# Optimization experiments

Measured on AMD Instinct MI355X. Metric: run time of the kernel, lower is better.

Reference implementation:

```python
import jax, jax.numpy as jnp
import numpy as np

N, IN, H, M, D = 2048, 400, 256, 128, 8


def setup_inputs() -> dict:
    key = jax.random.key(0)
    ks = jax.random.split(key, 20)
    g = lambda k, shp, s: jax.random.normal(k, shp, jnp.float32) * s
    C = IN // 2
    return {
        "x": g(ks[0], (N, IN), 1.0),
        "memory": g(ks[1], (N, H, M), 1.0),
        "ke_w": g(ks[2], (H, C), 1.0 / np.sqrt(C)),
        "ke_b": g(ks[3], (H,), 0.01),
        "km_w": g(ks[4], (M, H), 1.0 / np.sqrt(H)),
        "km_b": g(ks[5], (M,), 0.01),
        "kw2_w": g(ks[6], (D, H), 1.0 / np.sqrt(H)),
        "kw2_b": g(ks[7], (D,), 0.01),
        "sum_w": g(ks[8], (H, 2 * H), 1.0 / np.sqrt(2 * H)),
        "sum_b": g(ks[9], (H,), 0.01),
        "out_w": g(ks[10], (1, H), 1.0 / np.sqrt(H)),
        "out_b": g(ks[11], (1,), 0.01),
        "ve_w": g(ks[12], (H, IN), 1.0 / np.sqrt(IN)),
        "ve_b": g(ks[13], (H,), 0.01),
        "er_w": g(ks[14], (D, H, H), 1.0 / np.sqrt(H)),
        "er_b": g(ks[15], (D, H), 0.01),
        "ad_w": g(ks[16], (D, H, H), 1.0 / np.sqrt(H)),
        "ad_b": g(ks[17], (D, H), 0.01),
    }


def reference(x, memory, ke_w, ke_b, km_w, km_b, kw2_w, kw2_b,
              sum_w, sum_b, out_w, out_b, ve_w, ve_b,
              er_w, er_b, ad_w, ad_b):
    n, c2 = x.shape
    c = c2 // 2
    # query = sum of the two halves of x
    q = x.reshape(n, 2, c).sum(axis=1)                       # (N, C)
    k = q @ ke_w.T + ke_b                                    # (N, H)
    w = jax.nn.softmax(k @ km_w.T + km_b, axis=-1)           # (N, M) read/write weights
    w2 = jax.nn.softmax(k @ kw2_w.T + kw2_b, axis=-1)        # (N, D) expert gates
    # memory read: weighted sum over memory slots
    r = jnp.einsum('nhm,nm->nh', memory, w)                  # (N, H)
    f = jnp.tanh(jnp.concatenate([k, r], axis=1) @ sum_w.T + sum_b)
    y = f @ out_w.T + out_b                                  # (N, 1)
    v = x @ ve_w.T + ve_b                                    # (N, H)
    # DynamicLinear: gate-weighted mixture of per-expert linear maps
    # (fused: avoids materializing per-sample (N,H,H) weights)
    e = jax.nn.sigmoid(jnp.einsum('ni,doi,nd->no', v, er_w, w2) + w2 @ er_b)
    a = jnp.tanh(jnp.einsum('ni,doi,nd->no', v, ad_w, w2) + w2 @ ad_b)
    # memory write: erase then add
    memory = memory * (1.0 - w[:, None, :] * e[:, :, None])
    memory = memory + w[:, None, :] * a[:, :, None]
    return y, memory
```

## Files before the change

### kernel.cpp

```cpp
#include <hip/hip_runtime.h>
#include <math.h>

#define N_  2048
#define IN_ 400
#define C_  200
#define H_  256
#define M_  128
#define D_  8

#define KQ   224
#define KX   416
#define KBIG 2176
#define NZ   4
#define KSPL (KBIG / NZ)
#define KS   512

typedef __bf16 bf16x8 __attribute__((ext_vector_type(8)));
typedef float  f32x4  __attribute__((ext_vector_type(4)));

__device__ __forceinline__ ushort f2bf(float x) { __bf16 b = (__bf16)x; return __builtin_bit_cast(ushort, b); }
__device__ __forceinline__ float  bf2f(ushort u) { unsigned v = ((unsigned)u) << 16; return __builtin_bit_cast(float, v); }

#define P0 212992
#define P1 (P0 + 114688)
#define P2 (P1 + 81920)
#define P3 (P2 + 278528)
#define WC_KE (256 * KQ)
#define WC_VE (WC_KE + 256 * KX)
#define WC_SW (WC_VE + 256 * 512)
#define WC_KM (WC_SW + 128 * 256)
__global__ __launch_bounds__(256) void prep_all_kernel(
    const float* __restrict__ x,
    const float* __restrict__ ke, const float* __restrict__ ve,
    const float* __restrict__ sw, const float* __restrict__ km,
    const float* __restrict__ er_w, const float* __restrict__ er_b,
    const float* __restrict__ ad_w, const float* __restrict__ ad_b,
    ushort* __restrict__ x_bf, ushort* __restrict__ q_bf,
    ushort* __restrict__ wout, ushort* __restrict__ wcat)
{
    int idx = blockIdx.x * 256 + threadIdx.x;
    ushort pk[4];
    if (idx < P0) {
        int n = idx / (KX / 4), g = idx % (KX / 4), c0 = g * 4;
#pragma unroll
        for (int j = 0; j < 4; j++) {
            int c = c0 + j;
            pk[j] = f2bf((c < IN_) ? x[(size_t)n * IN_ + c] : 0.f);
        }
        *(ushort4*)&x_bf[(size_t)n * KX + c0] = *(ushort4*)pk;
    } else if (idx < P1) {
        int i = idx - P0;
        int n = i / (KQ / 4), g = i % (KQ / 4), c0 = g * 4;
#pragma unroll
        for (int j = 0; j < 4; j++) {
            int c = c0 + j;
            pk[j] = f2bf((c < C_) ? x[(size_t)n * IN_ + c] + x[(size_t)n * IN_ + C_ + c] : 0.f);
        }
        *(ushort4*)&q_bf[(size_t)n * KQ + c0] = *(ushort4*)pk;
    } else if (idx < P2) {
        int s0 = (idx - P1) * 4;
#pragma unroll
        for (int j = 0; j < 4; j++) {
            int s = s0 + j;
            float val;
            if (s < WC_KE)      { int r = s / KQ, c = s % KQ; val = (c < C_) ? ke[r * C_ + c] : 0.f; }
            else if (s < WC_VE) { int i = s - WC_KE; int r = i / KX, c = i % KX; val = (c < IN_) ? ve[r * IN_ + c] : 0.f; }
            else if (s < WC_SW) { val = sw[s - WC_VE]; }
            else                { val = km[s - WC_SW]; }
            pk[j] = f2bf(val);
        }
        *(ushort4*)&wout[s0] = *(ushort4*)pk;
    } else {
        int i = idx - P2;
        int o = i / (KBIG / 4), g = i % (KBIG / 4), c0 = g * 4;
        const float* Wsrc = (o < 256) ? er_w : ad_w;
        const float* bsrc = (o < 256) ? er_b : ad_b;
        int oo = o & 255;
#pragma unroll
        for (int j = 0; j < 4; j++) {
            int c = c0 + j;
            float val = 0.f;
            if (c < 2048)      { int d = c >> 8, ii = c & 255; val = Wsrc[(size_t)(d * 256 + oo) * 256 + ii]; }
            else if (c < 2056) { val = bsrc[(c - 2048) * 256 + oo]; }
            pk[j] = f2bf(val);
        }
        *(ushort4*)&wcat[(size_t)o * KBIG + c0] = *(ushort4*)pk;
    }
}

template<int ACT, int OUTBF>
__global__ __launch_bounds__(256) void gemm_mfma(
    const ushort* __restrict__ A, int lda,
    const ushort* __restrict__ B, int ldb,
    const float* __restrict__ bias,
    void* __restrict__ Cv, int ldc, size_t csplit, int ksplit)
{
    constexpr int BM = 128, BN = 64;
    __shared__ ushort As[BM][40];
    __shared__ ushort Bs[BN][40];
    const int tid = threadIdx.x, lane = tid & 63, wave = tid >> 6;
    const int wm = (wave >> 1) * 64, wn = (wave & 1) * 32;
    const int m0 = blockIdx.y * BM, n0 = blockIdx.x * BN;
    const int kFrom = blockIdx.z * ksplit, kTo = kFrom + ksplit;

    f32x4 acc[4][2] = {};
    const int sr = tid >> 2;
    const int sc = (tid & 3) * 8;

    for (int k0 = kFrom; k0 < kTo; k0 += 32) {
        uint4 a0 = *(const uint4*)&A[(size_t)(m0 + sr) * lda + k0 + sc];
        uint4 a1 = *(const uint4*)&A[(size_t)(m0 + sr + 64) * lda + k0 + sc];
        uint4 b0 = *(const uint4*)&B[(size_t)(n0 + sr) * ldb + k0 + sc];
        *(uint4*)&As[sr][sc] = a0;
        *(uint4*)&As[sr + 64][sc] = a1;
        *(uint4*)&Bs[sr][sc] = b0;
        __syncthreads();

        const int ko = (lane >> 4) * 8;
        bf16x8 af[4], bfr[2];
#pragma unroll
        for (int i = 0; i < 4; i++)
            af[i] = __builtin_bit_cast(bf16x8, *(const uint4*)&As[wm + i * 16 + (lane & 15)][ko]);
#pragma unroll
        for (int j = 0; j < 2; j++)
            bfr[j] = __builtin_bit_cast(bf16x8, *(const uint4*)&Bs[wn + j * 16 + (lane & 15)][ko]);
#pragma unroll
        for (int i = 0; i < 4; i++)
#pragma unroll
            for (int j = 0; j < 2; j++)
                acc[i][j] = __builtin_amdgcn_mfma_f32_16x16x32_bf16(af[i], bfr[j], acc[i][j], 0, 0, 0);
        __syncthreads();
    }

    float* Cf = (float*)Cv + blockIdx.z * csplit;
    ushort* Cb = (ushort*)Cv;
#pragma unroll
    for (int i = 0; i < 4; i++) {
#pragma unroll
        for (int j = 0; j < 2; j++) {
            int row = m0 + wm + i * 16 + (lane >> 4) * 4;
            int col = n0 + wn + j * 16 + (lane & 15);
#pragma unroll
            for (int r = 0; r < 4; r++) {
                float val = acc[i][j][r];
                if (bias) val += bias[col];
                if (ACT == 1) val = tanhf(val);
                if (OUTBF) Cb[(size_t)(row + r) * ldc + col] = f2bf(val);
                else       Cf[(size_t)(row + r) * ldc + col] = val;
            }
        }
    }
}

__global__ __launch_bounds__(256) void vw_kernel(
    const ushort* __restrict__ kr, const float* __restrict__ v,
    const float* __restrict__ kw2_w, const float* __restrict__ kw2_b,
    ushort* __restrict__ vw)
{
    __shared__ float kf[H_], vl[H_], lg[8], w2l[8];
    const int n = blockIdx.x, t = threadIdx.x;
    if (t < 64) {
        ushort4 u = ((const ushort4*)(kr + (size_t)n * KS))[t];
        kf[t * 4 + 0] = bf2f(u.x); kf[t * 4 + 1] = bf2f(u.y);
        kf[t * 4 + 2] = bf2f(u.z); kf[t * 4 + 3] = bf2f(u.w);
        float4 vv = ((const float4*)(v + (size_t)n * H_))[t];
        vl[t * 4 + 0] = vv.x; vl[t * 4 + 1] = vv.y;
        vl[t * 4 + 2] = vv.z; vl[t * 4 + 3] = vv.w;
    }
    __syncthreads();
    {
        int d = t >> 5, l = t & 31;
        float acc = 0.f;
        const float* wr = kw2_w + d * H_;
#pragma unroll
        for (int s = 0; s < 8; s++) acc += kf[l + 32 * s] * wr[l + 32 * s];
#pragma unroll
        for (int off = 16; off; off >>= 1) acc += __shfl_xor(acc, off);
        if (l == 0) lg[d] = acc + kw2_b[d];
    }
    __syncthreads();
    if (t < 8) {
        float val = lg[t];
        float mx = val;
#pragma unroll
        for (int off = 1; off < 8; off <<= 1) mx = fmaxf(mx, __shfl_xor(mx, off));
        float e = expf(val - mx), s = e;
#pragma unroll
        for (int off = 1; off < 8; off <<= 1) s += __shfl_xor(s, off);
        w2l[t] = e / s;
    }
    __syncthreads();
    ushort* row = vw + (size_t)n * KBIG;
    for (int g = t; g < KBIG / 4; g += 256) {
        int c0 = g * 4;
        ushort pk[4];
#pragma unroll
        for (int j = 0; j < 4; j++) {
            int c = c0 + j;
            float val = 0.f;
            if (c < 2048)      val = w2l[c >> 8] * vl[c & 255];
            else if (c < 2056) val = w2l[c - 2048];
            pk[j] = f2bf(val);
        }
        *(ushort4*)&row[c0] = *(ushort4*)pk;
    }
}

__global__ __launch_bounds__(256) void mem_stream_kernel(
    const float* __restrict__ mem_in,
    const float* __restrict__ wlog,
    const float* __restrict__ parts,
    float* __restrict__ mem_out,
    ushort* __restrict__ kr)
{
    __shared__ float wl[M_];
    __shared__ float el[128], al[128];
    __shared__ float red[4];
    const int n = blockIdx.x >> 1, half = blockIdx.x & 1, hbase = half * 128;
    const int t = threadIdx.x;

    const int col = (t < 128) ? (hbase + t) : (256 + hbase + (t - 128));
    float pacc = 0.f;
#pragma unroll
    for (int z = 0; z < NZ; z++)
        pacc += parts[(size_t)z * N_ * 512 + (size_t)n * 512 + col];

    float lv = 0.f;
    if (t < 128) {
        lv = wlog[(size_t)n * M_ + t];
        float mx = lv;
#pragma unroll
        for (int off = 32; off; off >>= 1) mx = fmaxf(mx, __shfl_xor(mx, off));
        if ((t & 63) == 0) red[t >> 6] = mx;
        el[t] = 1.f / (1.f + expf(-pacc));
    } else {
        al[t - 128] = tanhf(pacc);
    }
    __syncthreads();
    if (t < 128) {
        float gmax = fmaxf(red[0], red[1]);
        float ev = expf(lv - gmax);
        float s = ev;
#pragma unroll
        for (int off = 32; off; off >>= 1) s += __shfl_xor(s, off);
        if ((t & 63) == 0) red[2 + (t >> 6)] = s;
        wl[t] = ev;
    }
    __syncthreads();
    if (t < 128) wl[t] *= 1.f / (red[2] + red[3]);
    __syncthreads();

    const int wave = t >> 6, lane = t & 63, half2 = lane >> 5, l32 = lane & 31;
    const float4* min4 = (const float4*)(mem_in + ((size_t)n * H_ + hbase) * M_);
    float4* mout4 = (float4*)(mem_out + ((size_t)n * H_ + hbase) * M_);
    float4 wv = ((const float4*)wl)[l32];
#pragma unroll 4
    for (int i = 0; i < 16; i++) {
        int hl = i * 8 + wave * 2 + half2;
        float4 mv = min4[hl * 32 + l32];
        float eh = el[hl], ah = al[hl];
        float4 nv;
        nv.x = mv.x * (1.f - wv.x * eh) + wv.x * ah;
        nv.y = mv.y * (1.f - wv.y * eh) + wv.y * ah;
        nv.z = mv.z * (1.f - wv.z * eh) + wv.z * ah;
        nv.w = mv.w * (1.f - wv.w * eh) + wv.w * ah;
        mout4[hl * 32 + l32] = nv;
        float racc = mv.x * wv.x + mv.y * wv.y + mv.z * wv.z + mv.w * wv.w;
#pragma unroll
        for (int off = 1; off < 32; off <<= 1) racc += __shfl_xor(racc, off);
        if (l32 == 0) kr[(size_t)n * KS + H_ + hbase + hl] = f2bf(racc);
    }
}

__global__ void y_kernel(const float* __restrict__ f, const float* __restrict__ out_w,
                         const float* __restrict__ out_b, float* __restrict__ y) {
    int n = blockIdx.x, t = threadIdx.x;
    float acc = 0.f;
#pragma unroll
    for (int j = 0; j < 4; j++) acc += f[(size_t)n * H_ + t + j * 64] * out_w[t + j * 64];
#pragma unroll
    for (int off = 32; off; off >>= 1) acc += __shfl_xor(acc, off);
    if (t == 0) y[n] = acc + out_b[0];
}

extern "C" void kernel_launch(void* const* d_in, const int* in_sizes, int n_in,
                              void* d_out, int out_size, void* d_ws, size_t ws_size,
                              hipStream_t stream) {
    const float* x      = (const float*)d_in[0];
    const float* mem_in = (const float*)d_in[1];
    const float* ke_w   = (const float*)d_in[2];
    const float* ke_b   = (const float*)d_in[3];
    const float* km_w   = (const float*)d_in[4];
    const float* km_b   = (const float*)d_in[5];
    const float* kw2_w  = (const float*)d_in[6];
    const float* kw2_b  = (const float*)d_in[7];
    const float* sum_w  = (const float*)d_in[8];
    const float* sum_b  = (const float*)d_in[9];
    const float* out_w  = (const float*)d_in[10];
    const float* out_b  = (const float*)d_in[11];
    const float* ve_w   = (const float*)d_in[12];
    const float* ve_b   = (const float*)d_in[13];
    const float* er_w   = (const float*)d_in[14];
    const float* er_b   = (const float*)d_in[15];
    const float* ad_w   = (const float*)d_in[16];
    const float* ad_b   = (const float*)d_in[17];

    float* y_out   = (float*)d_out;
    float* mem_out = (float*)d_out + N_;

    float* ws = (float*)d_ws;
    size_t o = 0;
    float*  parts  = ws + o;            o += (size_t)NZ * N_ * 512;
    ushort* vw     = (ushort*)(ws + o); o += (size_t)N_ * KBIG / 2;
    ushort* Wcat   = (ushort*)(ws + o); o += (size_t)512 * KBIG / 2;
    ushort* kr     = (ushort*)(ws + o); o += (size_t)N_ * KS / 2;
    ushort* x_bf   = (ushort*)(ws + o); o += (size_t)N_ * KX / 2;
    ushort* q_bf   = (ushort*)(ws + o); o += (size_t)N_ * KQ / 2;
    ushort* wbf    = (ushort*)(ws + o); o += (size_t)WC_KM / 2;
    float*  v      = ws + o;            o += (size_t)N_ * H_;
    float*  wlog   = ws + o;            o += (size_t)N_ * M_;
    float*  fbuf   = (float*)x_bf;

    ushort* ke_bf  = wbf;
    ushort* ve_bf  = wbf + WC_KE;
    ushort* sum_bf = wbf + WC_VE;
    ushort* km_bf  = wbf + WC_SW;

    prep_all_kernel<<<P3 / 256, 256, 0, stream>>>(
        x, ke_w, ve_w, sum_w, km_w, er_w, er_b, ad_w, ad_b, x_bf, q_bf, wbf, Wcat);
    gemm_mfma<0, 1><<<dim3(H_ / 64, N_ / 128, 1), 256, 0, stream>>>(
        q_bf, KQ, ke_bf, KQ, ke_b, kr, KS, 0, KQ);
    gemm_mfma<0, 0><<<dim3(H_ / 64, N_ / 128, 1), 256, 0, stream>>>(
        x_bf, KX, ve_bf, KX, ve_b, v, H_, 0, KX);
    vw_kernel<<<N_, 256, 0, stream>>>(kr, v, kw2_w, kw2_b, vw);
    gemm_mfma<0, 0><<<dim3(512 / 64, N_ / 128, NZ), 256, 0, stream>>>(
        vw, KBIG, Wcat, KBIG, nullptr, parts, 512, (size_t)N_ * 512, KSPL);
    gemm_mfma<0, 0><<<dim3(M_ / 64, N_ / 128, 1), 256, 0, stream>>>(
        kr, KS, km_bf, H_, km_b, wlog, M_, 0, H_);
    mem_stream_kernel<<<2 * N_, 256, 0, stream>>>(mem_in, wlog, parts, mem_out, kr);
    gemm_mfma<1, 0><<<dim3(H_ / 64, N_ / 128, 1), 256, 0, stream>>>(
        kr, KS, sum_bf, KS, sum_b, fbuf, H_, 0, KS);
    y_kernel<<<N_, 64, 0, stream>>>(fbuf, out_w, out_b, y_out);
}
```

Before: 203.6 us.

## Double-buffer GEMM core, merge GEMM launches, fuse sum-GEMM with output head

Moves the MFMA GEMM into a shared device function with double-buffered LDS tiles, so global loads for the next K-slice overlap compute on the current one. The ke/ve GEMMs share one launch, the big expert GEMM shares one with the km logits GEMM, and the sum GEMM is fused with tanh and the out_w dot into a single kernel that writes y directly. The memory-stream kernel switches to vector math with nontemporal loads and stores. This cuts launch count and the intermediate f buffer, at the cost of more LDS per block and some idle z-slice blocks in the merged launch.

```diff
diff --git a/kernel.cpp b/kernel.cpp
--- a/kernel.cpp
+++ b/kernel.cpp
@@ -88,51 +88,59 @@
     }
 }
 
-template<int ACT, int OUTBF>
-__global__ __launch_bounds__(256) void gemm_mfma(
+__device__ __forceinline__ void gemm_core_128x64(
     const ushort* __restrict__ A, int lda,
     const ushort* __restrict__ B, int ldb,
     const float* __restrict__ bias,
-    void* __restrict__ Cv, int ldc, size_t csplit, int ksplit)
-{
-    constexpr int BM = 128, BN = 64;
-    __shared__ ushort As[BM][40];
-    __shared__ ushort Bs[BN][40];
+    void* __restrict__ Cv, int ldc, int outbf,
+    int m0, int n0, int kFrom, int kTo,
+    ushort (*As)[128][40], ushort (*Bs)[64][40])
+{
     const int tid = threadIdx.x, lane = tid & 63, wave = tid >> 6;
     const int wm = (wave >> 1) * 64, wn = (wave & 1) * 32;
-    const int m0 = blockIdx.y * BM, n0 = blockIdx.x * BN;
-    const int kFrom = blockIdx.z * ksplit, kTo = kFrom + ksplit;
+    const int sr = tid >> 2, sc = (tid & 3) * 8;
 
     f32x4 acc[4][2] = {};
-    const int sr = tid >> 2;
-    const int sc = (tid & 3) * 8;
-
-    for (int k0 = kFrom; k0 < kTo; k0 += 32) {
-        uint4 a0 = *(const uint4*)&A[(size_t)(m0 + sr) * lda + k0 + sc];
-        uint4 a1 = *(const uint4*)&A[(size_t)(m0 + sr + 64) * lda + k0 + sc];
-        uint4 b0 = *(const uint4*)&B[(size_t)(n0 + sr) * ldb + k0 + sc];
-        *(uint4*)&As[sr][sc] = a0;
-        *(uint4*)&As[sr + 64][sc] = a1;
-        *(uint4*)&Bs[sr][sc] = b0;
-        __syncthreads();
-
+
+    auto compute = [&](int b) {
         const int ko = (lane >> 4) * 8;
         bf16x8 af[4], bfr[2];
 #pragma unroll
         for (int i = 0; i < 4; i++)
-            af[i] = __builtin_bit_cast(bf16x8, *(const uint4*)&As[wm + i * 16 + (lane & 15)][ko]);
+            af[i] = __builtin_bit_cast(bf16x8, *(const uint4*)&As[b][wm + i * 16 + (lane & 15)][ko]);
 #pragma unroll
         for (int j = 0; j < 2; j++)
-            bfr[j] = __builtin_bit_cast(bf16x8, *(const uint4*)&Bs[wn + j * 16 + (lane & 15)][ko]);
+            bfr[j] = __builtin_bit_cast(bf16x8, *(const uint4*)&Bs[b][wn + j * 16 + (lane & 15)][ko]);
 #pragma unroll
         for (int i = 0; i < 4; i++)
 #pragma unroll
             for (int j = 0; j < 2; j++)
                 acc[i][j] = __builtin_amdgcn_mfma_f32_16x16x32_bf16(af[i], bfr[j], acc[i][j], 0, 0, 0);
+    };
+
+    uint4 a0 = *(const uint4*)&A[(size_t)(m0 + sr) * lda + kFrom + sc];
+    uint4 a1 = *(const uint4*)&A[(size_t)(m0 + sr + 64) * lda + kFrom + sc];
+    uint4 b0 = *(const uint4*)&B[(size_t)(n0 + sr) * ldb + kFrom + sc];
+    *(uint4*)&As[0][sr][sc] = a0;
+    *(uint4*)&As[0][sr + 64][sc] = a1;
+    *(uint4*)&Bs[0][sr][sc] = b0;
+    __syncthreads();
+
+    int cur = 0;
+    for (int k0 = kFrom + 32; k0 < kTo; k0 += 32) {
+        a0 = *(const uint4*)&A[(size_t)(m0 + sr) * lda + k0 + sc];
+        a1 = *(const uint4*)&A[(size_t)(m0 + sr + 64) * lda + k0 + sc];
+        b0 = *(const uint4*)&B[(size_t)(n0 + sr) * ldb + k0 + sc];
+        compute(cur);
+        *(uint4*)&As[cur ^ 1][sr][sc] = a0;
+        *(uint4*)&As[cur ^ 1][sr + 64][sc] = a1;
+        *(uint4*)&Bs[cur ^ 1][sr][sc] = b0;
         __syncthreads();
-    }
-
-    float* Cf = (float*)Cv + blockIdx.z * csplit;
+        cur ^= 1;
+    }
+    compute(cur);
+
+    float* Cf = (float*)Cv;
     ushort* Cb = (ushort*)Cv;
 #pragma unroll
     for (int i = 0; i < 4; i++) {
@@ -144,11 +152,46 @@
             for (int r = 0; r < 4; r++) {
                 float val = acc[i][j][r];
                 if (bias) val += bias[col];
-                if (ACT == 1) val = tanhf(val);
-                if (OUTBF) Cb[(size_t)(row + r) * ldc + col] = f2bf(val);
+                if (outbf) Cb[(size_t)(row + r) * ldc + col] = f2bf(val);
                 else       Cf[(size_t)(row + r) * ldc + col] = val;
             }
         }
+    }
+}
+
+__global__ __launch_bounds__(256) void kv_kernel(
+    const ushort* __restrict__ q_bf, const ushort* __restrict__ ke_bf,
+    const float* __restrict__ ke_b, ushort* __restrict__ kr,
+    const ushort* __restrict__ x_bf, const ushort* __restrict__ ve_bf,
+    const float* __restrict__ ve_b, float* __restrict__ v)
+{
+    __shared__ ushort As[2][128][40];
+    __shared__ ushort Bs[2][64][40];
+    if (blockIdx.z == 0)
+        gemm_core_128x64(q_bf, KQ, ke_bf, KQ, ke_b, kr, KS, 1,
+                         blockIdx.y * 128, blockIdx.x * 64, 0, KQ, As, Bs);
+    else
+        gemm_core_128x64(x_bf, KX, ve_bf, KX, ve_b, v, H_, 0,
+                         blockIdx.y * 128, blockIdx.x * 64, 0, KX, As, Bs);
+}
+
+__global__ __launch_bounds__(256) void bigw_kernel(
+    const ushort* __restrict__ vw, const ushort* __restrict__ Wcat,
+    float* __restrict__ parts,
+    const ushort* __restrict__ kr, const ushort* __restrict__ km_bf,
+    const float* __restrict__ km_b, float* __restrict__ wlog)
+{
+    __shared__ ushort As[2][128][40];
+    __shared__ ushort Bs[2][64][40];
+    const int z = blockIdx.z;
+    if (z < NZ) {
+        gemm_core_128x64(vw, KBIG, Wcat, KBIG, nullptr,
+                         parts + (size_t)z * N_ * 512, 512, 0,
+                         blockIdx.y * 128, blockIdx.x * 64, z * KSPL, (z + 1) * KSPL, As, Bs);
+    } else {
+        if (blockIdx.x >= 2) return;
+        gemm_core_128x64(kr, KS, km_bf, H_, km_b, wlog, M_, 0,
+                         blockIdx.y * 128, blockIdx.x * 64, 0, H_, As, Bs);
     }
 }
 
@@ -251,36 +294,119 @@
     __syncthreads();
 
     const int wave = t >> 6, lane = t & 63, half2 = lane >> 5, l32 = lane & 31;
-    const float4* min4 = (const float4*)(mem_in + ((size_t)n * H_ + hbase) * M_);
-    float4* mout4 = (float4*)(mem_out + ((size_t)n * H_ + hbase) * M_);
-    float4 wv = ((const float4*)wl)[l32];
+    const f32x4* min4 = (const f32x4*)(mem_in + ((size_t)n * H_ + hbase) * M_);
+    f32x4* mout4 = (f32x4*)(mem_out + ((size_t)n * H_ + hbase) * M_);
+    f32x4 wv = ((const f32x4*)wl)[l32];
 #pragma unroll 4
     for (int i = 0; i < 16; i++) {
         int hl = i * 8 + wave * 2 + half2;
-        float4 mv = min4[hl * 32 + l32];
+        f32x4 mv = __builtin_nontemporal_load(&min4[hl * 32 + l32]);
         float eh = el[hl], ah = al[hl];
-        float4 nv;
-        nv.x = mv.x * (1.f - wv.x * eh) + wv.x * ah;
-        nv.y = mv.y * (1.f - wv.y * eh) + wv.y * ah;
-        nv.z = mv.z * (1.f - wv.z * eh) + wv.z * ah;
-        nv.w = mv.w * (1.f - wv.w * eh) + wv.w * ah;
-        mout4[hl * 32 + l32] = nv;
-        float racc = mv.x * wv.x + mv.y * wv.y + mv.z * wv.z + mv.w * wv.w;
+        f32x4 nv = mv * (1.f - wv * eh) + wv * ah;
+        __builtin_nontemporal_store(nv, &mout4[hl * 32 + l32]);
+        float racc = mv[0] * wv[0] + mv[1] * wv[1] + mv[2] * wv[2] + mv[3] * wv[3];
 #pragma unroll
         for (int off = 1; off < 32; off <<= 1) racc += __shfl_xor(racc, off);
         if (l32 == 0) kr[(size_t)n * KS + H_ + hbase + hl] = f2bf(racc);
     }
 }
 
-__global__ void y_kernel(const float* __restrict__ f, const float* __restrict__ out_w,
-                         const float* __restrict__ out_b, float* __restrict__ y) {
-    int n = blockIdx.x, t = threadIdx.x;
-    float acc = 0.f;
-#pragma unroll
-    for (int j = 0; j < 4; j++) acc += f[(size_t)n * H_ + t + j * 64] * out_w[t + j * 64];
-#pragma unroll
-    for (int off = 32; off; off >>= 1) acc += __shfl_xor(acc, off);
-    if (t == 0) y[n] = acc + out_b[0];
+__global__ __launch_bounds__(256) void fy_kernel(
+    const ushort* __restrict__ kr, const ushort* __restrict__ sum_bf,
+    const float* __restrict__ sum_b, const float* __restrict__ out_w,
+    const float* __restrict__ out_b, float* __restrict__ y)
+{
+    __shared__ ushort As[2][64][40];
+    __shared__ ushort Bs[2][256][40];
+    __shared__ float yl[64][4];
+    const int tid = threadIdx.x, lane = tid & 63, wave = tid >> 6;
+    const int wn = wave * 64;
+    const int m0 = blockIdx.x * 64;
+    const int sr = tid >> 2, sc = (tid & 3) * 8;
+
+    f32x4 acc[4][4] = {};
+
+    auto compute = [&](int b) {
+        const int ko = (lane >> 4) * 8;
+        bf16x8 af[4], bfr[4];
+#pragma unroll
+        for (int i = 0; i < 4; i++)
+            af[i] = __builtin_bit_cast(bf16x8, *(const uint4*)&As[b][i * 16 + (lane & 15)][ko]);
+#pragma unroll
+        for (int j = 0; j < 4; j++)
+            bfr[j] = __builtin_bit_cast(bf16x8, *(const uint4*)&Bs[b][wn + j * 16 + (lane & 15)][ko]);
+#pragma unroll
+        for (int i = 0; i < 4; i++)
+#pragma unroll
+            for (int j = 0; j < 4; j++)
+                acc[i][j] = __builtin_amdgcn_mfma_f32_16x16x32_bf16(af[i], bfr[j], acc[i][j], 0, 0, 0);
+    };
+
+    uint4 a0 = *(const uint4*)&kr[(size_t)(m0 + sr) * KS + 0 + sc];
+    uint4 b0 = *(const uint4*)&sum_bf[(size_t)(sr)       * KS + 0 + sc];
+    uint4 b1 = *(const uint4*)&sum_bf[(size_t)(sr + 64)  * KS + 0 + sc];
+    uint4 b2 = *(const uint4*)&sum_bf[(size_t)(sr + 128) * KS + 0 + sc];
+    uint4 b3 = *(const uint4*)&sum_bf[(size_t)(sr + 192) * KS + 0 + sc];
+    *(uint4*)&As[0][sr][sc] = a0;
+    *(uint4*)&Bs[0][sr][sc] = b0;
+    *(uint4*)&Bs[0][sr + 64][sc] = b1;
+    *(uint4*)&Bs[0][sr + 128][sc] = b2;
+    *(uint4*)&Bs[0][sr + 192][sc] = b3;
+    __syncthreads();
+
+    int cur = 0;
+    for (int k0 = 32; k0 < KS; k0 += 32) {
+        a0 = *(const uint4*)&kr[(size_t)(m0 + sr) * KS + k0 + sc];
+        b0 = *(const uint4*)&sum_bf[(size_t)(sr)       * KS + k0 + sc];
+        b1 = *(const uint4*)&sum_bf[(size_t)(sr + 64)  * KS + k0 + sc];
+        b2 = *(const uint4*)&sum_bf[(size_t)(sr + 128) * KS + k0 + sc];
+        b3 = *(const uint4*)&sum_bf[(size_t)(sr + 192) * KS + k0 + sc];
+        compute(cur);
+        *(uint4*)&As[cur ^ 1][sr][sc] = a0;
+        *(uint4*)&Bs[cur ^ 1][sr][sc] = b0;
+        *(uint4*)&Bs[cur ^ 1][sr + 64][sc] = b1;
+        *(uint4*)&Bs[cur ^ 1][sr + 128][sc] = b2;
+        *(uint4*)&Bs[cur ^ 1][sr + 192][sc] = b3;
+        __syncthreads();
+        cur ^= 1;
+    }
+    compute(cur);
+
+    float ow[4], sb[4];
+#pragma unroll
+    for (int j = 0; j < 4; j++) {
+        int col = wn + j * 16 + (lane & 15);
+        ow[j] = out_w[col];
+        sb[j] = sum_b[col];
+    }
+    float yp[4][4];
+#pragma unroll
+    for (int i = 0; i < 4; i++)
+#pragma unroll
+        for (int r = 0; r < 4; r++) {
+            float s = 0.f;
+#pragma unroll
+            for (int j = 0; j < 4; j++)
+                s += tanhf(acc[i][j][r] + sb[j]) * ow[j];
+            yp[i][r] = s;
+        }
+#pragma unroll
+    for (int off = 1; off < 16; off <<= 1)
+#pragma unroll
+        for (int i = 0; i < 4; i++)
+#pragma unroll
+            for (int r = 0; r < 4; r++)
+                yp[i][r] += __shfl_xor(yp[i][r], off);
+    if ((lane & 15) == 0) {
+#pragma unroll
+        for (int i = 0; i < 4; i++)
+#pragma unroll
+            for (int r = 0; r < 4; r++)
+                yl[i * 16 + (lane >> 4) * 4 + r][wave] = yp[i][r];
+    }
+    __syncthreads();
+    if (tid < 64)
+        y[m0 + tid] = yl[tid][0] + yl[tid][1] + yl[tid][2] + yl[tid][3] + out_b[0];
 }
 
 extern "C" void kernel_launch(void* const* d_in, const int* in_sizes, int n_in,
@@ -319,7 +445,6 @@
     ushort* wbf    = (ushort*)(ws + o); o += (size_t)WC_KM / 2;
     float*  v      = ws + o;            o += (size_t)N_ * H_;
     float*  wlog   = ws + o;            o += (size_t)N_ * M_;
-    float*  fbuf   = (float*)x_bf;
 
     ushort* ke_bf  = wbf;
     ushort* ve_bf  = wbf + WC_KE;
@@ -328,17 +453,11 @@
 
     prep_all_kernel<<<P3 / 256, 256, 0, stream>>>(
         x, ke_w, ve_w, sum_w, km_w, er_w, er_b, ad_w, ad_b, x_bf, q_bf, wbf, Wcat);
-    gemm_mfma<0, 1><<<dim3(H_ / 64, N_ / 128, 1), 256, 0, stream>>>(
-        q_bf, KQ, ke_bf, KQ, ke_b, kr, KS, 0, KQ);
-    gemm_mfma<0, 0><<<dim3(H_ / 64, N_ / 128, 1), 256, 0, stream>>>(
-        x_bf, KX, ve_bf, KX, ve_b, v, H_, 0, KX);
+    kv_kernel<<<dim3(4, 16, 2), 256, 0, stream>>>(
+        q_bf, ke_bf, ke_b, kr, x_bf, ve_bf, ve_b, v);
     vw_kernel<<<N_, 256, 0, stream>>>(kr, v, kw2_w, kw2_b, vw);
-    gemm_mfma<0, 0><<<dim3(512 / 64, N_ / 128, NZ), 256, 0, stream>>>(
-        vw, KBIG, Wcat, KBIG, nullptr, parts, 512, (size_t)N_ * 512, KSPL);
-    gemm_mfma<0, 0><<<dim3(M_ / 64, N_ / 128, 1), 256, 0, stream>>>(
-        kr, KS, km_bf, H_, km_b, wlog, M_, 0, H_);
+    bigw_kernel<<<dim3(8, 16, NZ + 1), 256, 0, stream>>>(
+        vw, Wcat, parts, kr, km_bf, km_b, wlog);
     mem_stream_kernel<<<2 * N_, 256, 0, stream>>>(mem_in, wlog, parts, mem_out, kr);
-    gemm_mfma<1, 0><<<dim3(H_ / 64, N_ / 128, 1), 256, 0, stream>>>(
-        kr, KS, sum_bf, KS, sum_b, fbuf, H_, 0, KS);
-    y_kernel<<<N_, 64, 0, stream>>>(fbuf, out_w, out_b, y_out);
-}
+    fy_kernel<<<N_ / 64, 256, 0, stream>>>(kr, sum_bf, sum_b, out_w, out_b, y_out);
+}
```

After: 170.4 us. 1.19x faster.
